# Performance work log

Measured on AMD Instinct MI355X. Metric: run time of the kernel, lower is better.

Reference implementation:

```python
import jax, jax.numpy as jnp
import numpy as np

VTH = 1.0      # v_threshold
TAU = 2.0      # spikingjelly LIFNode default tau
ALPHA = 2.0    # ATan surrogate alpha
EPS = 1e-5     # BatchNorm eps
N_HEADS = 8
TOPK = 4       # routed regions per query region
REGION = 64    # tokens per region (4096 tokens -> 64 regions)


@jax.custom_vjp
def spike_fn(v):
    return (v >= VTH).astype(v.dtype)

def _spike_fwd(v):
    return (v >= VTH).astype(v.dtype), v

def _spike_bwd(v, g):
    sg = (ALPHA / 2.0) / (1.0 + (jnp.pi / 2.0 * ALPHA * (v - VTH)) ** 2)
    return (g * sg,)

spike_fn.defvjp(_spike_fwd, _spike_bwd)


def lif(x):
    # x: [T, B, L, D]; LIF with decay_input=True, hard reset to 0, detach_reset
    def step(v, xt):
        v = v + (xt - v) / TAU
        s = spike_fn(v)
        v = v * (1.0 - jax.lax.stop_gradient(s))
        return v, s
    _, s = jax.lax.scan(step, jnp.zeros_like(x[0]), x)
    return s


def batchnorm(x, gamma, beta):
    # torch BN1d over [T*B, D, L] in training mode == per-channel stats over (T,B,L)
    mean = x.mean(axis=(0, 1, 2))
    var = jnp.mean((x - mean) ** 2, axis=(0, 1, 2))
    return (x - mean) * jax.lax.rsqrt(var + EPS) * gamma + beta


def bilevel_attn(x, qkv_w, qkv_b, proj_w, proj_b):
    # x: [TB, L, D]
    TB, L, D = x.shape
    nreg = L // REGION
    hd = D // N_HEADS
    qkv = x @ qkv_w.T + qkv_b
    q, k, v = jnp.split(qkv, 3, axis=-1)
    qr = q.reshape(TB, nreg, REGION, D)
    kr = k.reshape(TB, nreg, REGION, D)
    vr = v.reshape(TB, nreg, REGION, D)
    # coarse region-level routing via mean-pooled q/k affinity
    aff = jnp.einsum('bnd,bmd->bnm', qr.mean(2), kr.mean(2))  # [TB, nreg, nreg]
    _, idx = jax.lax.top_k(aff, TOPK)                         # [TB, nreg, TOPK]
    gather = jax.vmap(lambda t, ix: t[ix])                    # per-sample region gather
    kg = gather(kr, idx).reshape(TB, nreg, TOPK * REGION, N_HEADS, hd)
    vg = gather(vr, idx).reshape(TB, nreg, TOPK * REGION, N_HEADS, hd)
    qh = qr.reshape(TB, nreg, REGION, N_HEADS, hd)
    logits = jnp.einsum('bnqhd,bnkhd->bnhqk', qh, kg) * (hd ** -0.5)
    p = jax.nn.softmax(logits, axis=-1)
    o = jnp.einsum('bnhqk,bnkhd->bnqhd', p, vg).reshape(TB, L, D)
    return o @ proj_w.T + proj_b


def setup_inputs() -> dict:
    key = jax.random.key(0)
    ks = jax.random.split(key, 8)
    T, B, Lt, L, D = 4, 2, 4, 1024, 256
    Ltot = Lt * L
    s = 0.02
    return {
        'x': jax.random.normal(ks[0], (T, B, Ltot, D), jnp.float32),
        'bn1_g': jnp.ones((D,), jnp.float32),
        'bn1_b': jnp.zeros((D,), jnp.float32),
        'bn2_g': jnp.ones((D,), jnp.float32),
        'bn2_b': jnp.zeros((D,), jnp.float32),
        'qkv_w': jax.random.normal(ks[1], (3 * D, D), jnp.float32) * s,
        'qkv_b': jnp.zeros((3 * D,), jnp.float32),
        'proj_w': jax.random.normal(ks[2], (D, D), jnp.float32) * s,
        'proj_b': jnp.zeros((D,), jnp.float32),
        'ffn_w1': jax.random.normal(ks[3], (4 * D, D), jnp.float32) * s,
        'ffn_b1': jnp.zeros((4 * D,), jnp.float32),
        'ffn_w2': jax.random.normal(ks[4], (D, 4 * D), jnp.float32) * s,
        'ffn_b2': jnp.zeros((D,), jnp.float32),
        'scale': jnp.ones((1,), jnp.float32) * 0.5,
        'Lt': Lt, 'b': B, 'L': L, 'dim': D,
    }


def reference(x, bn1_g, bn1_b, bn2_g, bn2_b, qkv_w, qkv_b, proj_w, proj_b,
              ffn_w1, ffn_b1, ffn_w2, ffn_b2, scale, Lt, b, L, dim):
    T = x.shape[0]
    Ltot = Lt * L
    # attention branch
    identity = x
    s1 = lif(batchnorm(x, bn1_g, bn1_b))
    a = bilevel_attn(s1.reshape(T * b, Ltot, dim), qkv_w, qkv_b, proj_w, proj_b)
    x = identity + a.reshape(T, b, Ltot, dim) * scale
    # ffn branch
    s2 = lif(batchnorm(x, bn2_g, bn2_b))
    h = jax.nn.gelu(s2 @ ffn_w1.T + ffn_b1, approximate=False) @ ffn_w2.T + ffn_b2
    return x + h * scale
```

## Files before the change

kernel.cpp:

```cpp
#include <hip/hip_runtime.h>
#include <hip/hip_bf16.h>
#include <math.h>

typedef __attribute__((ext_vector_type(8))) short short8;
typedef __attribute__((ext_vector_type(4))) float f32x4;

#define DIM 256
#define NROWS 32768
#define PERT 2097152
#define SAMP_TOK 4096

__device__ __forceinline__ float b2f(__hip_bfloat16 h){ return __bfloat162float(h); }
__device__ __forceinline__ __hip_bfloat16 f2b(float f){ return __float2bfloat16(f); }
__device__ __forceinline__ unsigned short f2bu(float f){
  __hip_bfloat16 h = __float2bfloat16(f);
  unsigned short u; __builtin_memcpy(&u, &h, 2); return u;
}

#define GLD_LDS16(gp, lp) __builtin_amdgcn_global_load_lds( \
    (const __attribute__((address_space(1))) unsigned int*)(gp), \
    (__attribute__((address_space(3))) unsigned int*)(lp), 16, 0, 0)

__device__ __forceinline__ float gelu_fast(float v){
  float z  = v * 0.70710678118654752f;
  float az = fabsf(z);
  float t  = __builtin_amdgcn_rcpf(fmaf(0.3275911f, az, 1.0f));
  float p  = fmaf(fmaf(fmaf(fmaf(1.061405429f, t, -1.453152027f), t,
                            1.421413741f), t, -0.284496736f), t, 0.254829592f);
  p *= t;
  float e  = __expf(-z * z);
  float y  = fmaf(-p, e, 1.0f);
  return fmaf(0.5f * fabsf(v), y, 0.5f * v);
}

__global__ void f2ball_k(const float* __restrict__ w_qkv, const float* __restrict__ w_proj,
                         const float* __restrict__ w_f1, const float* __restrict__ w_f2,
                         __hip_bfloat16* __restrict__ o_qkv, __hip_bfloat16* __restrict__ o_proj,
                         __hip_bfloat16* __restrict__ o_f1, __hip_bfloat16* __restrict__ o_f2){
  int i = blockIdx.x * 256 + threadIdx.x;
  if (i < 196608)          o_qkv[i]           = f2b(w_qkv[i]);
  else if (i < 262144)     o_proj[i - 196608] = f2b(w_proj[i - 196608]);
  else if (i < 524288)     o_f1[i - 262144]   = f2b(w_f1[i - 262144]);
  else                     o_f2[i - 524288]   = f2b(w_f2[i - 524288]);
}

__global__ void bn_stats_k(const float* __restrict__ x, float* __restrict__ sum, float* __restrict__ sumsq){
  __shared__ __align__(16) float rs[4][256];
  __shared__ __align__(16) float rq[4][256];
  int t = threadIdx.x;
  int g = t & 63, r = t >> 6;
  size_t base = ((size_t)blockIdx.x * 128 + r) * DIM + g * 4;
  float4 s = {0.f,0.f,0.f,0.f}, q = {0.f,0.f,0.f,0.f};
  for (int i = 0; i < 32; ++i){
    float4 v = *reinterpret_cast<const float4*>(x + base + (size_t)i * 4 * DIM);
    s.x += v.x; s.y += v.y; s.z += v.z; s.w += v.w;
    q.x += v.x*v.x; q.y += v.y*v.y; q.z += v.z*v.z; q.w += v.w*v.w;
  }
  *reinterpret_cast<float4*>(&rs[r][g*4]) = s;
  *reinterpret_cast<float4*>(&rq[r][g*4]) = q;
  __syncthreads();
  int c = t;
  atomicAdd(&sum[c],   rs[0][c] + rs[1][c] + rs[2][c] + rs[3][c]);
  atomicAdd(&sumsq[c], rq[0][c] + rq[1][c] + rq[2][c] + rq[3][c]);
}

__global__ void bn_fin_k(const float* __restrict__ sum, const float* __restrict__ sumsq,
                         const float* __restrict__ g, const float* __restrict__ b,
                         float* __restrict__ a_out, float* __restrict__ b_out){
  int c = threadIdx.x;
  float mean = sum[c] * (1.f/32768.f);
  float var  = sumsq[c] * (1.f/32768.f) - mean*mean;
  float a = g[c] / sqrtf(var + 1e-5f);
  a_out[c] = a;
  b_out[c] = b[c] - mean * a;
}

__global__ void bn_red_k(const float* __restrict__ pps, const float* __restrict__ ppq,
                         const float* __restrict__ g, const float* __restrict__ b,
                         float* __restrict__ a_out, float* __restrict__ b_out){
  int c = threadIdx.x;
  float s = 0.f, q = 0.f;
  for (int r = 0; r < 512; ++r){
    s += pps[r * 256 + c];
    q += ppq[r * 256 + c];
  }
  float mean = s * (1.f/32768.f);
  float var  = q * (1.f/32768.f) - mean*mean;
  float a = g[c] / sqrtf(var + 1e-5f);
  a_out[c] = a;
  b_out[c] = b[c] - mean * a;
}

__global__ void lif_k(const float* __restrict__ x, const float* __restrict__ av,
                      const float* __restrict__ bv, __hip_bfloat16* __restrict__ s){
  int i = blockIdx.x * 256 + threadIdx.x;
  int e4 = i * 4;
  int c4 = e4 & (DIM - 1);
  float4 a = *reinterpret_cast<const float4*>(av + c4);
  float4 b = *reinterpret_cast<const float4*>(bv + c4);
  float4 v = {0.f,0.f,0.f,0.f};
  #pragma unroll
  for (int t = 0; t < 4; ++t){
    float4 xn = *reinterpret_cast<const float4*>(x + (size_t)t * PERT + e4);
    xn.x = fmaf(xn.x, a.x, b.x); xn.y = fmaf(xn.y, a.y, b.y);
    xn.z = fmaf(xn.z, a.z, b.z); xn.w = fmaf(xn.w, a.w, b.w);
    v.x += (xn.x - v.x) * 0.5f; v.y += (xn.y - v.y) * 0.5f;
    v.z += (xn.z - v.z) * 0.5f; v.w += (xn.w - v.w) * 0.5f;
    ushort4 sp;
    sp.x = (v.x >= 1.0f) ? 0x3F80 : 0;  v.x = (v.x >= 1.0f) ? 0.f : v.x;
    sp.y = (v.y >= 1.0f) ? 0x3F80 : 0;  v.y = (v.y >= 1.0f) ? 0.f : v.y;
    sp.z = (v.z >= 1.0f) ? 0x3F80 : 0;  v.z = (v.z >= 1.0f) ? 0.f : v.z;
    sp.w = (v.w >= 1.0f) ? 0x3F80 : 0;  v.w = (v.w >= 1.0f) ? 0.f : v.w;
    *reinterpret_cast<ushort4*>(reinterpret_cast<unsigned short*>(s) + (size_t)t * PERT + e4) = sp;
  }
}

__global__ void region_sum_k(const __hip_bfloat16* __restrict__ s, float* __restrict__ sm){
  __shared__ __align__(16) float red[4][256];
  int r = blockIdx.x, t = threadIdx.x;
  int g = t & 63, sub = t >> 6;
  const unsigned short* sp = reinterpret_cast<const unsigned short*>(s);
  size_t base = ((size_t)r * 64 + sub * 16) * DIM + g * 4;
  float4 acc = {0.f,0.f,0.f,0.f};
  for (int i = 0; i < 16; ++i){
    ushort4 u = *reinterpret_cast<const ushort4*>(sp + base + (size_t)i * DIM);
    acc.x += (u.x != 0) ? 1.f : 0.f; acc.y += (u.y != 0) ? 1.f : 0.f;
    acc.z += (u.z != 0) ? 1.f : 0.f; acc.w += (u.w != 0) ? 1.f : 0.f;
  }
  *reinterpret_cast<float4*>(&red[sub][g*4]) = acc;
  __syncthreads();
  if (sub == 0){
    float4 o;
    o.x = (red[0][g*4+0] + red[1][g*4+0] + red[2][g*4+0] + red[3][g*4+0]) * 0.015625f;
    o.y = (red[0][g*4+1] + red[1][g*4+1] + red[2][g*4+1] + red[3][g*4+1]) * 0.015625f;
    o.z = (red[0][g*4+2] + red[1][g*4+2] + red[2][g*4+2] + red[3][g*4+2]) * 0.015625f;
    o.w = (red[0][g*4+3] + red[1][g*4+3] + red[2][g*4+3] + red[3][g*4+3]) * 0.015625f;
    *reinterpret_cast<float4*>(sm + (size_t)r * DIM + g * 4) = o;
  }
}

__global__ void rgemm_k(const float* __restrict__ smr, const float* __restrict__ w,
                        const float* __restrict__ bias, float* __restrict__ qkm){
  __shared__ float arow[256];
  int r = blockIdx.x, t = threadIdx.x;
  arow[t] = smr[(size_t)r * 256 + t];
  __syncthreads();
  for (int j = t; j < 512; j += 256){
    const float* wr = w + (size_t)j * 256;
    float acc = 0.f;
    for (int k = 0; k < 256; ++k) acc += arow[k] * wr[k];
    qkm[(size_t)r * 512 + j] = acc + bias[j];
  }
}

template<int EPI>
__global__ __launch_bounds__(256) void gemm_bt(
    const __hip_bfloat16* __restrict__ A, const __hip_bfloat16* __restrict__ W,
    const float* __restrict__ bias, void* __restrict__ outp,
    const void* __restrict__ extra, const float* __restrict__ scaleptr,
    float* __restrict__ pps, float* __restrict__ ppq,
    int K, int N)
{
  __shared__ __align__(16) short As0[128 * 32];
  __shared__ __align__(16) short Ws0[128 * 32];
  __shared__ __align__(16) short As1[128 * 32];
  __shared__ __align__(16) short Ws1[128 * 32];
  int tid = threadIdx.x;
  int bm = blockIdx.x, bn = blockIdx.y;
  int lane = tid & 63;
  int l16 = lane & 15, quad = lane >> 4;
  int wv = tid >> 6;
  int wm = (wv >> 1) << 6, wn = (wv & 1) << 6;

  const int srow = tid >> 2;
  const int sq   = (tid & 3) ^ ((srow >> 1) & 3);
  const __hip_bfloat16* Ag = A + (size_t)(bm * 128 + srow) * K + (sq << 3);
  const __hip_bfloat16* Wg = W + (size_t)(bn * 128 + srow) * K + (sq << 3);
  const size_t rstep = (size_t)64 * K;

  int roA[4], roW[4];
  #pragma unroll
  for (int i = 0; i < 4; ++i){
    int Ra = wm + i * 16 + l16;
    roA[i] = Ra * 32 + ((quad ^ ((Ra >> 1) & 3)) << 3);
    int Rw = wn + i * 16 + l16;
    roW[i] = Rw * 32 + ((quad ^ ((Rw >> 1) & 3)) << 3);
  }

  f32x4 zero = {0.f, 0.f, 0.f, 0.f};
  f32x4 acc[4][4];
  #pragma unroll
  for (int i = 0; i < 4; ++i)
    #pragma unroll
    for (int j = 0; j < 4; ++j) acc[i][j] = zero;

  auto stage = [&](short* Ad, short* Wd, int k0){
    GLD_LDS16(Ag + k0,         Ad + tid * 8);
    GLD_LDS16(Ag + rstep + k0, Ad + tid * 8 + 2048);
    GLD_LDS16(Wg + k0,         Wd + tid * 8);
    GLD_LDS16(Wg + rstep + k0, Wd + tid * 8 + 2048);
  };
  auto compute = [&](const short* Asb, const short* Wsb){
    short8 af[4];
    #pragma unroll
    for (int mi = 0; mi < 4; ++mi)
      af[mi] = *reinterpret_cast<const short8*>(Asb + roA[mi]);
    #pragma unroll
    for (int ni = 0; ni < 4; ++ni){
      short8 wf = *reinterpret_cast<const short8*>(Wsb + roW[ni]);
      #pragma unroll
      for (int mi = 0; mi < 4; ++mi)
        acc[mi][ni] = __builtin_amdgcn_mfma_f32_16x16x32_bf16(wf, af[mi], acc[mi][ni], 0, 0, 0);
    }
  };

  stage(As0, Ws0, 0);
  __syncthreads();
  for (int k0 = 0; k0 < K; k0 += 64){
    if (k0 + 32 < K) stage(As1, Ws1, k0 + 32);
    compute(As0, Ws0);
    __syncthreads();
    if (k0 + 64 < K) stage(As0, Ws0, k0 + 64);
    if (k0 + 32 < K) compute(As1, Ws1);
    __syncthreads();
  }

  if (EPI == 0 || EPI == 2){
    short* Cw = (wv == 0) ? As0 : (wv == 1) ? Ws0 : (wv == 2) ? As1 : Ws1;
    #pragma unroll
    for (int ni = 0; ni < 4; ++ni){
      int col0 = (bn << 7) + wn + ni * 16 + (quad << 2);
      float4 bv = *reinterpret_cast<const float4*>(bias + col0);
      #pragma unroll
      for (int mi = 0; mi < 4; ++mi){
        float v0 = acc[mi][ni][0] + bv.x;
        float v1 = acc[mi][ni][1] + bv.y;
        float v2 = acc[mi][ni][2] + bv.z;
        float v3 = acc[mi][ni][3] + bv.w;
        if (EPI == 2){
          v0 = gelu_fast(v0); v1 = gelu_fast(v1);
          v2 = gelu_fast(v2); v3 = gelu_fast(v3);
        }
        unsigned lo = (unsigned)f2bu(v0) | ((unsigned)f2bu(v1) << 16);
        unsigned hi = (unsigned)f2bu(v2) | ((unsigned)f2bu(v3) << 16);
        int row = mi * 16 + l16;
        int cb  = (ni * 32 + (quad << 3)) ^ ((row & 7) << 4);
        *reinterpret_cast<uint2*>(reinterpret_cast<char*>(Cw) + row * 128 + cb) =
            make_uint2(lo, hi);
      }
    }
    asm volatile("s_waitcnt lgkmcnt(0)" ::: "memory");
    #pragma unroll
    for (int p = 0; p < 8; ++p){
      int row = p * 8 + (lane >> 3);
      int cb  = ((lane & 7) << 4) ^ ((row & 7) << 4);
      uint4 val = *reinterpret_cast<const uint4*>(
          reinterpret_cast<const char*>(Cw) + row * 128 + cb);
      int rowg = (bm << 7) + wm + row;
      int colg = (bn << 7) + wn + ((lane & 7) << 3);
      *reinterpret_cast<uint4*>((__hip_bfloat16*)outp + (size_t)rowg * N + colg) = val;
    }
  } else {
    float sc = scaleptr[0];
    float4 ts[4], tq[4];
    if (EPI == 1){
      #pragma unroll
      for (int ni = 0; ni < 4; ++ni){ ts[ni] = {0.f,0.f,0.f,0.f}; tq[ni] = {0.f,0.f,0.f,0.f}; }
    }
    #pragma unroll
    for (int ni = 0; ni < 4; ++ni){
      int col0 = (bn << 7) + wn + ni * 16 + (quad << 2);
      float4 bv = *reinterpret_cast<const float4*>(bias + col0);
      #pragma unroll
      for (int mi = 0; mi < 4; ++mi){
        int rowg = (bm << 7) + wm + mi * 16 + l16;
        size_t off = (size_t)rowg * N + col0;
        float v0 = acc[mi][ni][0] + bv.x;
        float v1 = acc[mi][ni][1] + bv.y;
        float v2 = acc[mi][ni][2] + bv.z;
        float v3 = acc[mi][ni][3] + bv.w;
        float4 xr = *reinterpret_cast<const float4*>((const float*)extra + off);
        float4 ov;
        ov.x = xr.x + v0 * sc; ov.y = xr.y + v1 * sc;
        ov.z = xr.z + v2 * sc; ov.w = xr.w + v3 * sc;
        *reinterpret_cast<float4*>((float*)outp + off) = ov;
        if (EPI == 1){
          ts[ni].x += ov.x; ts[ni].y += ov.y; ts[ni].z += ov.z; ts[ni].w += ov.w;
          tq[ni].x += ov.x*ov.x; tq[ni].y += ov.y*ov.y;
          tq[ni].z += ov.z*ov.z; tq[ni].w += ov.w*ov.w;
        }
      }
    }
    if (EPI == 1){
      int prow = (bm << 1) + (wm >> 6);
      #pragma unroll
      for (int ni = 0; ni < 4; ++ni){
        float4 S = ts[ni], Q = tq[ni];
        #pragma unroll
        for (int m = 1; m < 16; m <<= 1){
          S.x += __shfl_xor(S.x, m); S.y += __shfl_xor(S.y, m);
          S.z += __shfl_xor(S.z, m); S.w += __shfl_xor(S.w, m);
          Q.x += __shfl_xor(Q.x, m); Q.y += __shfl_xor(Q.y, m);
          Q.z += __shfl_xor(Q.z, m); Q.w += __shfl_xor(Q.w, m);
        }
        if (l16 == 0){
          int col0 = (bn << 7) + wn + ni * 16 + (quad << 2);
          *reinterpret_cast<float4*>(pps + prow * 256 + col0) = S;
          *reinterpret_cast<float4*>(ppq + prow * 256 + col0) = Q;
        }
      }
    }
  }
}

__global__ void topk_k(const float* __restrict__ qkm, int* __restrict__ idx){
  __shared__ float aff[64];
  int r = blockIdx.x;
  int m = threadIdx.x;
  int b = r >> 6;
  const float4* qrow = reinterpret_cast<const float4*>(qkm + (size_t)r * 512);
  const float4* krow = reinterpret_cast<const float4*>(qkm + (size_t)(b * 64 + m) * 512 + 256);
  float dot = 0.f;
  for (int d = 0; d < 64; ++d){
    float4 qv = qrow[d], kv = krow[d];
    dot += qv.x * kv.x + qv.y * kv.y + qv.z * kv.z + qv.w * kv.w;
  }
  aff[m] = dot;
  __syncthreads();
  if (m == 0){
    #pragma unroll
    for (int t = 0; t < 4; ++t){
      float best = -INFINITY; int bi = 0;
      for (int i = 0; i < 64; ++i){
        if (aff[i] > best){ best = aff[i]; bi = i; }
      }
      aff[bi] = -INFINITY;
      idx[r * 4 + t] = bi;
    }
  }
}

__global__ __launch_bounds__(256) void attn_mfma_k(
    const __hip_bfloat16* __restrict__ qkv, const int* __restrict__ idx,
    __hip_bfloat16* __restrict__ o_out, int rbase)
{
  __shared__ __align__(16) short lds[27136];
  const int rl = blockIdx.x;
  const int h  = blockIdx.y;
  const int rg = rbase + rl;
  const int bl = rl >> 6;
  const int tid = threadIdx.x;
  const int w = tid >> 6, lane = tid & 63;
  const int l16 = lane & 15, quad = lane >> 4;
  short* Pw = lds + 10240 + w * 4224;

  const int reg = idx[rg * 4 + (tid >> 6)] & 63;
  const size_t srow = (size_t)bl * SAMP_TOK + (size_t)reg * 64 + (tid & 63);
  const __hip_bfloat16* kvsrc = qkv + srow * 768 + 256 + (size_t)h * 32;

  const size_t qrow = (size_t)rl * 64 + w * 16 + l16;
  short8 qf = *reinterpret_cast<const short8*>(qkv + qrow * 768 + (size_t)h * 32 + quad * 8);

  uint4 vreg[4];
  #pragma unroll
  for (int c = 0; c < 4; ++c)
    vreg[c] = *reinterpret_cast<const uint4*>(kvsrc + 256 + c * 8);

  #pragma unroll
  for (int c = 0; c < 4; ++c)
    *reinterpret_cast<uint4*>(&lds[tid * 40 + c * 8]) =
      *reinterpret_cast<const uint4*>(kvsrc + c * 8);
  __syncthreads();

  f32x4 s[16];
  #pragma unroll
  for (int nt = 0; nt < 16; ++nt){
    short8 kf = *reinterpret_cast<const short8*>(&lds[(nt * 16 + l16) * 40 + quad * 8]);
    f32x4 z = {0.f, 0.f, 0.f, 0.f};
    s[nt] = __builtin_amdgcn_mfma_f32_16x16x32_bf16(kf, qf, z, 0, 0, 0);
  }
  __syncthreads();

  #pragma unroll
  for (int c = 0; c < 4; ++c){
    short8 vv = *reinterpret_cast<short8*>(&vreg[c]);
    #pragma unroll
    for (int e = 0; e < 8; ++e)
      lds[(c * 8 + e) * 264 + tid] = vv[e];
  }

  float mx = -1e30f;
  #pragma unroll
  for (int nt = 0; nt < 16; ++nt)
    #pragma unroll
    for (int r = 0; r < 4; ++r) mx = fmaxf(mx, s[nt][r]);
  mx = fmaxf(mx, __shfl_xor(mx, 16));
  mx = fmaxf(mx, __shfl_xor(mx, 32));
  float den = 0.f;
  #pragma unroll
  for (int nt = 0; nt < 16; ++nt)
    #pragma unroll
    for (int r = 0; r < 4; ++r){
      float e = __expf((s[nt][r] - mx) * 0.17677669529663687f);
      s[nt][r] = e; den += e;
    }
  den += __shfl_xor(den, 16);
  den += __shfl_xor(den, 32);

  #pragma unroll
  for (int nt = 0; nt < 16; ++nt){
    unsigned lo = (unsigned)f2bu(s[nt][0]) | ((unsigned)f2bu(s[nt][1]) << 16);
    unsigned hi = (unsigned)f2bu(s[nt][2]) | ((unsigned)f2bu(s[nt][3]) << 16);
    *reinterpret_cast<uint2*>(&Pw[l16 * 264 + nt * 16 + quad * 4]) = make_uint2(lo, hi);
  }
  __syncthreads();

  f32x4 o0 = {0.f, 0.f, 0.f, 0.f}, o1 = o0;
  #pragma unroll
  for (int kk = 0; kk < 8; ++kk){
    short8 pb = *reinterpret_cast<const short8*>(&Pw[l16 * 264 + kk * 32 + quad * 8]);
    short8 a0 = *reinterpret_cast<const short8*>(&lds[l16 * 264 + kk * 32 + quad * 8]);
    short8 a1 = *reinterpret_cast<const short8*>(&lds[(16 + l16) * 264 + kk * 32 + quad * 8]);
    o0 = __builtin_amdgcn_mfma_f32_16x16x32_bf16(a0, pb, o0, 0, 0, 0);
    o1 = __builtin_amdgcn_mfma_f32_16x16x32_bf16(a1, pb, o1, 0, 0, 0);
  }
  float inv = 1.f / den;
  size_t obase = ((size_t)rl * 64 + w * 16 + l16) * 256 + (size_t)h * 32;
  unsigned pk0 = (unsigned)f2bu(o0[0] * inv) | ((unsigned)f2bu(o0[1] * inv) << 16);
  unsigned pk1 = (unsigned)f2bu(o0[2] * inv) | ((unsigned)f2bu(o0[3] * inv) << 16);
  unsigned pk2 = (unsigned)f2bu(o1[0] * inv) | ((unsigned)f2bu(o1[1] * inv) << 16);
  unsigned pk3 = (unsigned)f2bu(o1[2] * inv) | ((unsigned)f2bu(o1[3] * inv) << 16);
  *reinterpret_cast<uint2*>(o_out + obase + quad * 4)      = make_uint2(pk0, pk1);
  *reinterpret_cast<uint2*>(o_out + obase + 16 + quad * 4) = make_uint2(pk2, pk3);
}

extern "C" void kernel_launch(void* const* d_in, const int* in_sizes, int n_in,
                              void* d_out, int out_size, void* d_ws, size_t ws_size,
                              hipStream_t stream)
{
  const float* x      = (const float*)d_in[0];
  const float* bn1_g  = (const float*)d_in[1];
  const float* bn1_b  = (const float*)d_in[2];
  const float* bn2_g  = (const float*)d_in[3];
  const float* bn2_b  = (const float*)d_in[4];
  const float* qkv_w  = (const float*)d_in[5];
  const float* qkv_b  = (const float*)d_in[6];
  const float* proj_w = (const float*)d_in[7];
  const float* proj_b = (const float*)d_in[8];
  const float* ffn_w1 = (const float*)d_in[9];
  const float* ffn_b1 = (const float*)d_in[10];
  const float* ffn_w2 = (const float*)d_in[11];
  const float* ffn_b2 = (const float*)d_in[12];
  const float* scale  = (const float*)d_in[13];
  float* x2 = (float*)d_out;

  char* ws = (char*)d_ws;
  const size_t MB = 1024 * 1024;
  float* sum1 = (float*)(ws + 0);
  float* sq1  = (float*)(ws + 1024);
  float* a1   = (float*)(ws + 4096);
  float* b1   = (float*)(ws + 5120);
  float* a2   = (float*)(ws + 6144);
  float* b2   = (float*)(ws + 7168);
  int*   idxb = (int*)(ws + 8192);
  float* smr  = (float*)(ws + 16384);
  float* qkm  = (float*)(ws + 540672);
  __hip_bfloat16* qkv_wb  = (__hip_bfloat16*)(ws + 1589248);
  __hip_bfloat16* proj_wb = (__hip_bfloat16*)(ws + 1982464);
  __hip_bfloat16* ffn_w1b = (__hip_bfloat16*)(ws + 2113536);
  __hip_bfloat16* ffn_w2b = (__hip_bfloat16*)(ws + 2637824);
  float* ppsum = (float*)(ws + 3162112);
  float* ppsq  = (float*)(ws + 3686400);
  __hip_bfloat16* s1 = (__hip_bfloat16*)(ws + 4 * MB);
  __hip_bfloat16* s2 = s1;
  char* chunkbuf = ws + 20 * MB;

  size_t avail = (ws_size > 20 * MB) ? (ws_size - 20 * MB) : (8 * MB);
  int nc = (avail >= 64 * MB) ? 8 : (avail >= 32 * MB) ? 4 : (avail >= 16 * MB) ? 2 : 1;
  int crows = 32768;
  while ((size_t)crows * 2048 > avail && crows > 2048) crows >>= 1;

  __hip_bfloat16* qkvc = (__hip_bfloat16*)chunkbuf;
  __hip_bfloat16* oc   = (__hip_bfloat16*)(chunkbuf + (size_t)nc * 6 * MB);
  __hip_bfloat16* h1   = (__hip_bfloat16*)chunkbuf;

  hipMemsetAsync(d_ws, 0, 4096, stream);

  f2ball_k<<<3072, 256, 0, stream>>>(qkv_w, proj_w, ffn_w1, ffn_w2,
                                     qkv_wb, proj_wb, ffn_w1b, ffn_w2b);

  bn_stats_k<<<256, 256, 0, stream>>>(x, sum1, sq1);
  bn_fin_k<<<1, 256, 0, stream>>>(sum1, sq1, bn1_g, bn1_b, a1, b1);
  lif_k<<<PERT / 1024, 256, 0, stream>>>(x, a1, b1, s1);
  region_sum_k<<<512, 256, 0, stream>>>(s1, smr);
  rgemm_k<<<512, 256, 0, stream>>>(smr, qkv_w, qkv_b, qkm);
  topk_k<<<512, 64, 0, stream>>>(qkm, idxb);

  const int nchunkA = 8 / nc;
  for (int c = 0; c < nchunkA; ++c){
    const size_t ro = (size_t)c * nc * SAMP_TOK;
    gemm_bt<0><<<dim3(nc * SAMP_TOK / 128, 6), 256, 0, stream>>>(
        s1 + ro * 256, qkv_wb, qkv_b, qkvc, nullptr, nullptr, nullptr, nullptr, 256, 768);
    attn_mfma_k<<<dim3(nc * 64, 8), 256, 0, stream>>>(qkvc, idxb, oc, c * nc * 64);
    gemm_bt<1><<<dim3(nc * SAMP_TOK / 128, 2), 256, 0, stream>>>(
        oc, proj_wb, proj_b, x2 + ro * 256, x + ro * 256, scale,
        ppsum + (ro >> 6) * 256, ppsq + (ro >> 6) * 256, 256, 256);
  }

  bn_red_k<<<1, 256, 0, stream>>>(ppsum, ppsq, bn2_g, bn2_b, a2, b2);
  lif_k<<<PERT / 1024, 256, 0, stream>>>(x2, a2, b2, s2);
  const int nchunkF = 32768 / crows;
  for (int c = 0; c < nchunkF; ++c){
    const size_t ro = (size_t)c * crows;
    gemm_bt<2><<<dim3(crows / 128, 8), 256, 0, stream>>>(
        s2 + ro * 256, ffn_w1b, ffn_b1, h1, nullptr, nullptr, nullptr, nullptr, 256, 1024);
    gemm_bt<3><<<dim3(crows / 128, 2), 256, 0, stream>>>(
        h1, ffn_w2b, ffn_b2, x2 + ro * 256, x2 + ro * 256, scale, nullptr, nullptr, 1024, 256);
  }
}
```

Measured before the change: 371.1 us.

## Fuse FFN up-projection, GELU and down-projection into one kernel

Replaces the two chunked FFN GEMM launches with a single kernel. Each block handles 64 rows: it computes 128-column slices of the hidden layer, applies GELU, keeps the bf16 result in LDS, and accumulates straight into the down-projection output. This avoids writing and re-reading the 32768x1024 bf16 hidden tensor in global memory. In exchange it launches only 512 blocks with a large LDS footprint and more serial K-loop steps per block, and both weight matrices are re-streamed by every block. gemm_bt is simplified to drop the EPI==2 path.

```diff
diff --git a/kernel.cpp b/kernel.cpp
--- a/kernel.cpp
+++ b/kernel.cpp
@@ -225,7 +225,7 @@
     __syncthreads();
   }
 
-  if (EPI == 0 || EPI == 2){
+  if (EPI == 0){
     short* Cw = (wv == 0) ? As0 : (wv == 1) ? Ws0 : (wv == 2) ? As1 : Ws1;
     #pragma unroll
     for (int ni = 0; ni < 4; ++ni){
@@ -237,10 +237,6 @@
         float v1 = acc[mi][ni][1] + bv.y;
         float v2 = acc[mi][ni][2] + bv.z;
         float v3 = acc[mi][ni][3] + bv.w;
-        if (EPI == 2){
-          v0 = gelu_fast(v0); v1 = gelu_fast(v1);
-          v2 = gelu_fast(v2); v3 = gelu_fast(v3);
-        }
         unsigned lo = (unsigned)f2bu(v0) | ((unsigned)f2bu(v1) << 16);
         unsigned hi = (unsigned)f2bu(v2) | ((unsigned)f2bu(v3) << 16);
         int row = mi * 16 + l16;
@@ -263,10 +259,8 @@
   } else {
     float sc = scaleptr[0];
     float4 ts[4], tq[4];
-    if (EPI == 1){
-      #pragma unroll
-      for (int ni = 0; ni < 4; ++ni){ ts[ni] = {0.f,0.f,0.f,0.f}; tq[ni] = {0.f,0.f,0.f,0.f}; }
-    }
+    #pragma unroll
+    for (int ni = 0; ni < 4; ++ni){ ts[ni] = {0.f,0.f,0.f,0.f}; tq[ni] = {0.f,0.f,0.f,0.f}; }
     #pragma unroll
     for (int ni = 0; ni < 4; ++ni){
       int col0 = (bn << 7) + wn + ni * 16 + (quad << 2);
@@ -284,31 +278,171 @@
         ov.x = xr.x + v0 * sc; ov.y = xr.y + v1 * sc;
         ov.z = xr.z + v2 * sc; ov.w = xr.w + v3 * sc;
         *reinterpret_cast<float4*>((float*)outp + off) = ov;
-        if (EPI == 1){
-          ts[ni].x += ov.x; ts[ni].y += ov.y; ts[ni].z += ov.z; ts[ni].w += ov.w;
-          tq[ni].x += ov.x*ov.x; tq[ni].y += ov.y*ov.y;
-          tq[ni].z += ov.z*ov.z; tq[ni].w += ov.w*ov.w;
-        }
-      }
-    }
-    if (EPI == 1){
-      int prow = (bm << 1) + (wm >> 6);
+        ts[ni].x += ov.x; ts[ni].y += ov.y; ts[ni].z += ov.z; ts[ni].w += ov.w;
+        tq[ni].x += ov.x*ov.x; tq[ni].y += ov.y*ov.y;
+        tq[ni].z += ov.z*ov.z; tq[ni].w += ov.w*ov.w;
+      }
+    }
+    int prow = (bm << 1) + (wm >> 6);
+    #pragma unroll
+    for (int ni = 0; ni < 4; ++ni){
+      float4 S = ts[ni], Q = tq[ni];
+      #pragma unroll
+      for (int m = 1; m < 16; m <<= 1){
+        S.x += __shfl_xor(S.x, m); S.y += __shfl_xor(S.y, m);
+        S.z += __shfl_xor(S.z, m); S.w += __shfl_xor(S.w, m);
+        Q.x += __shfl_xor(Q.x, m); Q.y += __shfl_xor(Q.y, m);
+        Q.z += __shfl_xor(Q.z, m); Q.w += __shfl_xor(Q.w, m);
+      }
+      if (l16 == 0){
+        int col0 = (bn << 7) + wn + ni * 16 + (quad << 2);
+        *reinterpret_cast<float4*>(pps + prow * 256 + col0) = S;
+        *reinterpret_cast<float4*>(ppq + prow * 256 + col0) = Q;
+      }
+    }
+  }
+}
+
+__global__ __launch_bounds__(256) void ffn_fused_k(
+    const __hip_bfloat16* __restrict__ A,
+    const __hip_bfloat16* __restrict__ W1,
+    const float* __restrict__ b1,
+    const __hip_bfloat16* __restrict__ W2,
+    const float* __restrict__ b2,
+    float* __restrict__ x2,
+    const float* __restrict__ scaleptr)
+{
+  __shared__ __align__(16) short lds[24832];
+  const int tid = threadIdx.x;
+  const int bm = blockIdx.x;
+  const int lane = tid & 63;
+  const int l16 = lane & 15, quad = lane >> 4;
+  const int wv = tid >> 6;
+
+  const int srow = tid >> 2;
+  const int sq   = (tid & 3) ^ ((srow >> 1) & 3);
+  const __hip_bfloat16* Ag = A + (size_t)(bm * 64 + srow) * 256 + (sq << 3);
+
+  int roA[4], roH[4], roW1[2], roW2[4];
+  #pragma unroll
+  for (int mi = 0; mi < 4; ++mi){
+    int Ra = mi * 16 + l16;
+    roA[mi] = Ra * 32 + ((quad ^ ((Ra >> 1) & 3)) << 3);
+    roH[mi] = 16384 + Ra * 132 + (quad << 3);
+  }
+  #pragma unroll
+  for (int ni = 0; ni < 2; ++ni){
+    int Rw = wv * 32 + ni * 16 + l16;
+    roW1[ni] = Rw * 32 + ((quad ^ ((Rw >> 1) & 3)) << 3);
+  }
+  #pragma unroll
+  for (int ni = 0; ni < 4; ++ni){
+    int Rw = wv * 64 + ni * 16 + l16;
+    roW2[ni] = Rw * 32 + ((quad ^ ((Rw >> 1) & 3)) << 3);
+  }
+
+  f32x4 zero = {0.f, 0.f, 0.f, 0.f};
+  f32x4 acc2[4][4];
+  #pragma unroll
+  for (int i = 0; i < 4; ++i)
+    #pragma unroll
+    for (int j = 0; j < 4; ++j) acc2[i][j] = zero;
+
+  for (int c1 = 0; c1 < 8; ++c1){
+    f32x4 acc1[4][2];
+    #pragma unroll
+    for (int i = 0; i < 4; ++i){ acc1[i][0] = zero; acc1[i][1] = zero; }
+
+    const __hip_bfloat16* W1g = W1 + (size_t)(c1 * 128 + srow) * 256 + (sq << 3);
+
+    auto stage1 = [&](int off, int k0){
+      GLD_LDS16(Ag + k0,              lds + off + tid * 8);
+      GLD_LDS16(W1g + k0,             lds + off + 2048 + tid * 8);
+      GLD_LDS16(W1g + 64 * 256 + k0,  lds + off + 2048 + tid * 8 + 2048);
+    };
+    stage1(0, 0);
+    __syncthreads();
+    #pragma unroll
+    for (int k = 0; k < 8; ++k){
+      const int cur = (k & 1) ? 6144 : 0;
+      const int nxt = (k & 1) ? 0 : 6144;
+      if (k < 7) stage1(nxt, (k + 1) * 32);
+      short8 af[4];
+      #pragma unroll
+      for (int mi = 0; mi < 4; ++mi)
+        af[mi] = *reinterpret_cast<const short8*>(lds + cur + roA[mi]);
+      #pragma unroll
+      for (int ni = 0; ni < 2; ++ni){
+        short8 wf = *reinterpret_cast<const short8*>(lds + cur + 2048 + roW1[ni]);
+        #pragma unroll
+        for (int mi = 0; mi < 4; ++mi)
+          acc1[mi][ni] = __builtin_amdgcn_mfma_f32_16x16x32_bf16(wf, af[mi], acc1[mi][ni], 0, 0, 0);
+      }
+      __syncthreads();
+    }
+
+    auto stageW2 = [&](int off, int kk){
+      const __hip_bfloat16* p = W2 + (size_t)srow * 1024 + c1 * 128 + kk * 32 + (sq << 3);
+      #pragma unroll
+      for (int j = 0; j < 4; ++j)
+        GLD_LDS16(p + (size_t)j * 64 * 1024, lds + off + tid * 8 + j * 2048);
+    };
+    stageW2(0, 0);
+    #pragma unroll
+    for (int ni = 0; ni < 2; ++ni){
+      int colg = c1 * 128 + wv * 32 + ni * 16 + (quad << 2);
+      float4 bv = *reinterpret_cast<const float4*>(b1 + colg);
+      #pragma unroll
+      for (int mi = 0; mi < 4; ++mi){
+        float g0 = gelu_fast(acc1[mi][ni][0] + bv.x);
+        float g1 = gelu_fast(acc1[mi][ni][1] + bv.y);
+        float g2 = gelu_fast(acc1[mi][ni][2] + bv.z);
+        float g3 = gelu_fast(acc1[mi][ni][3] + bv.w);
+        unsigned lo = (unsigned)f2bu(g0) | ((unsigned)f2bu(g1) << 16);
+        unsigned hi = (unsigned)f2bu(g2) | ((unsigned)f2bu(g3) << 16);
+        *reinterpret_cast<uint2*>(
+            lds + 16384 + (mi * 16 + l16) * 132 + wv * 32 + ni * 16 + (quad << 2)) =
+            make_uint2(lo, hi);
+      }
+    }
+    __syncthreads();
+
+    #pragma unroll
+    for (int kk = 0; kk < 4; ++kk){
+      const int cur = (kk & 1) ? 8192 : 0;
+      const int nxt = (kk & 1) ? 0 : 8192;
+      if (kk < 3) stageW2(nxt, kk + 1);
+      short8 af[4];
+      #pragma unroll
+      for (int mi = 0; mi < 4; ++mi)
+        af[mi] = *reinterpret_cast<const short8*>(lds + roH[mi] + kk * 32);
       #pragma unroll
       for (int ni = 0; ni < 4; ++ni){
-        float4 S = ts[ni], Q = tq[ni];
+        short8 wf = *reinterpret_cast<const short8*>(lds + cur + roW2[ni]);
         #pragma unroll
-        for (int m = 1; m < 16; m <<= 1){
-          S.x += __shfl_xor(S.x, m); S.y += __shfl_xor(S.y, m);
-          S.z += __shfl_xor(S.z, m); S.w += __shfl_xor(S.w, m);
-          Q.x += __shfl_xor(Q.x, m); Q.y += __shfl_xor(Q.y, m);
-          Q.z += __shfl_xor(Q.z, m); Q.w += __shfl_xor(Q.w, m);
-        }
-        if (l16 == 0){
-          int col0 = (bn << 7) + wn + ni * 16 + (quad << 2);
-          *reinterpret_cast<float4*>(pps + prow * 256 + col0) = S;
-          *reinterpret_cast<float4*>(ppq + prow * 256 + col0) = Q;
-        }
-      }
+        for (int mi = 0; mi < 4; ++mi)
+          acc2[mi][ni] = __builtin_amdgcn_mfma_f32_16x16x32_bf16(wf, af[mi], acc2[mi][ni], 0, 0, 0);
+      }
+      __syncthreads();
+    }
+  }
+
+  float sc = scaleptr[0];
+  #pragma unroll
+  for (int ni = 0; ni < 4; ++ni){
+    int col0 = wv * 64 + ni * 16 + (quad << 2);
+    float4 bv = *reinterpret_cast<const float4*>(b2 + col0);
+    #pragma unroll
+    for (int mi = 0; mi < 4; ++mi){
+      int rowg = bm * 64 + mi * 16 + l16;
+      size_t off = (size_t)rowg * 256 + col0;
+      float4 xr = *reinterpret_cast<const float4*>(x2 + off);
+      float4 ov;
+      ov.x = xr.x + (acc2[mi][ni][0] + bv.x) * sc;
+      ov.y = xr.y + (acc2[mi][ni][1] + bv.y) * sc;
+      ov.z = xr.z + (acc2[mi][ni][2] + bv.z) * sc;
+      ov.w = xr.w + (acc2[mi][ni][3] + bv.w) * sc;
+      *reinterpret_cast<float4*>(x2 + off) = ov;
     }
   }
 }
@@ -477,12 +611,9 @@
 
   size_t avail = (ws_size > 20 * MB) ? (ws_size - 20 * MB) : (8 * MB);
   int nc = (avail >= 64 * MB) ? 8 : (avail >= 32 * MB) ? 4 : (avail >= 16 * MB) ? 2 : 1;
-  int crows = 32768;
-  while ((size_t)crows * 2048 > avail && crows > 2048) crows >>= 1;
 
   __hip_bfloat16* qkvc = (__hip_bfloat16*)chunkbuf;
   __hip_bfloat16* oc   = (__hip_bfloat16*)(chunkbuf + (size_t)nc * 6 * MB);
-  __hip_bfloat16* h1   = (__hip_bfloat16*)chunkbuf;
 
   hipMemsetAsync(d_ws, 0, 4096, stream);
 
@@ -509,12 +640,5 @@
 
   bn_red_k<<<1, 256, 0, stream>>>(ppsum, ppsq, bn2_g, bn2_b, a2, b2);
   lif_k<<<PERT / 1024, 256, 0, stream>>>(x2, a2, b2, s2);
-  const int nchunkF = 32768 / crows;
-  for (int c = 0; c < nchunkF; ++c){
-    const size_t ro = (size_t)c * crows;
-    gemm_bt<2><<<dim3(crows / 128, 8), 256, 0, stream>>>(
-        s2 + ro * 256, ffn_w1b, ffn_b1, h1, nullptr, nullptr, nullptr, nullptr, 256, 1024);
-    gemm_bt<3><<<dim3(crows / 128, 2), 256, 0, stream>>>(
-        h1, ffn_w2b, ffn_b2, x2 + ro * 256, x2 + ro * 256, scale, nullptr, nullptr, 1024, 256);
-  }
-}
+  ffn_fused_k<<<512, 256, 0, stream>>>(s2, ffn_w1b, ffn_b1, ffn_w2b, ffn_b2, x2, scale);
+}
```

Result: faster. 357.5 us (-3.7%).
